# Kernel optimization log

Measured on AMD Instinct MI355X. Metric: run time of the kernel, lower is better.

The kernel has to match this reference:

```python
import jax, jax.numpy as jnp
import numpy as np

# Canonical topology: root object with K arrays, each array has L number leaves.
# Weights are tied across paths (tie_weights_containers=tie_weights_primitives=True),
# NumberEmbedder runs in eval mode with initial buffers mean=0, sqmean=1 -> identity norm.

K, L, D = 8192, 128, 64


def setup_inputs() -> dict:
    key = jax.random.key(0)
    ks = jax.random.split(key, 16)
    s = 1.0 / np.sqrt(D)
    return {
        "x": jax.random.normal(ks[0], (K, L), dtype=jnp.float32),
        "W_num": jax.random.normal(ks[1], (D, 1), dtype=jnp.float32) * s,
        "b_num": jax.random.normal(ks[2], (D,), dtype=jnp.float32) * s,
        "W_ih": jax.random.normal(ks[3], (4 * D, 2 * D), dtype=jnp.float32) * s,
        "W_hh": jax.random.normal(ks[4], (4 * D, D), dtype=jnp.float32) * s,
        "b_ih": jax.random.normal(ks[5], (4 * D,), dtype=jnp.float32) * s,
        "b_hh": jax.random.normal(ks[6], (4 * D,), dtype=jnp.float32) * s,
        "W_aout": jax.random.normal(ks[7], (D, D), dtype=jnp.float32) * s,
        "b_aout": jax.random.normal(ks[8], (D,), dtype=jnp.float32) * s,
        "W_fh": jax.random.normal(ks[9], (D, D), dtype=jnp.float32) * s,
        "b_fh": jax.random.normal(ks[10], (D,), dtype=jnp.float32) * s,
        "W_iouh": jax.random.normal(ks[11], (3 * D, D), dtype=jnp.float32) * s,
        "b_iouh": jax.random.normal(ks[12], (3 * D,), dtype=jnp.float32) * s,
        "W_oout": jax.random.normal(ks[13], (D, D), dtype=jnp.float32) * s,
        "b_oout": jax.random.normal(ks[14], (D,), dtype=jnp.float32) * s,
    }


def _forward(x, W_num, b_num, W_ih, W_hh, b_ih, b_hh, W_aout, b_aout,
             W_fh, b_fh, W_iouh, b_iouh, W_oout, b_oout):
    d = W_hh.shape[1]
    # --- NumberEmbedder: Linear(1, d) on identity-normalized numbers; c = 0 ---
    emb = x[..., None] * W_num[:, 0] + b_num          # [K, L, d]
    xs = jnp.transpose(emb, (1, 0, 2))                # [L, K, d] time-major for scan
    # --- ArrayEmbedder: LSTMCell over children; input = cat(child_h, child_c) ---
    # child_c is identically zero, so only the first half of W_ih contributes.
    W_ih_h = W_ih[:, :d]                              # [4d, d]
    bias = b_ih + b_hh                                # [4d]

    def step(carry, x_t):
        h, c = carry
        gates = x_t @ W_ih_h.T + h @ W_hh.T + bias    # [K, 4d]
        i, f, g, o = jnp.split(gates, 4, axis=1)
        c2 = jax.nn.sigmoid(f) * c + jax.nn.sigmoid(i) * jnp.tanh(g)
        h2 = jax.nn.sigmoid(o) * jnp.tanh(c2)
        return (h2, c2), None

    h0 = jnp.zeros((x.shape[0], d), dtype=x.dtype)
    (h_arr, c_arr), _ = jax.lax.scan(step, (h0, h0), xs)
    h_hat = h_arr @ W_aout.T + b_aout                 # [K, d] array lout
    # --- ObjectEmbedder: child-sum TreeLSTM over the K array states ---
    f = h_hat @ W_fh.T + b_fh                         # [K, d]
    fc_sum = jnp.sum(jax.nn.sigmoid(f) * c_arr, axis=0, keepdims=True)  # [1, d]
    hs_bar = jnp.sum(h_hat, axis=0, keepdims=True)    # [1, d]
    iou = hs_bar @ W_iouh.T + b_iouh                  # [1, 3d]
    i, o, u = jnp.split(iou, 3, axis=1)
    c_obj = jax.nn.sigmoid(i) * jnp.tanh(u) + fc_sum
    h_obj = jax.nn.sigmoid(o) * jnp.tanh(c_obj)
    h_hat_obj = h_obj @ W_oout.T + b_oout             # [1, d] object lout
    # root forward returns cat(h, c)
    return jnp.concatenate([h_hat_obj, c_obj], axis=1)  # [1, 2d]


def reference(x, W_num, b_num, W_ih, W_hh, b_ih, b_hh, W_aout, b_aout,
              W_fh, b_fh, W_iouh, b_iouh, W_oout, b_oout):
    return _forward(x, W_num, b_num, W_ih, W_hh, b_ih, b_hh, W_aout, b_aout,
                    W_fh, b_fh, W_iouh, b_iouh, W_oout, b_oout)
```

## Files before the change

### kernel.cpp

```cpp
#include <hip/hip_runtime.h>
#include <cstddef>

#define D   64
#define L   128
#define NT  256
#define ROWS 16
#define XSS 132
#define HBS 72
#define NBLK 512
#define LOG2E 1.4426950408889634f

typedef __attribute__((ext_vector_type(8))) short short8;
typedef __attribute__((ext_vector_type(4))) float floatx4;

__device__ __forceinline__ float fast_rcp(float x) {
#if defined(__has_builtin)
#if __has_builtin(__builtin_amdgcn_rcpf)
  return __builtin_amdgcn_rcpf(x);
#else
  return 1.0f / x;
#endif
#else
  return 1.0f / x;
#endif
}
__device__ __forceinline__ float ex2(float x) {
#if defined(__has_builtin)
#if __has_builtin(__builtin_amdgcn_exp2f)
  return __builtin_amdgcn_exp2f(x);
#else
  return __builtin_exp2f(x);
#endif
#else
  return __builtin_exp2f(x);
#endif
}
__device__ __forceinline__ float sig_plain(float x) {
  return fast_rcp(1.0f + ex2(-LOG2E * x));
}
__device__ __forceinline__ float tanh2(float G) {
  return fmaf(2.0f, fast_rcp(1.0f + ex2(G)), -1.0f);
}
__device__ __forceinline__ unsigned short f2bf_rtne(float f) {
  unsigned int u = __float_as_uint(f);
  u += 0x7fffu + ((u >> 16) & 1u);
  return (unsigned short)(u >> 16);
}
__device__ __forceinline__ float bf2f(unsigned short s) {
  return __uint_as_float(((unsigned int)s) << 16);
}

__global__ __launch_bounds__(NT, 2)
void lstm_main(const float* __restrict__ x,
               const float* __restrict__ W_num,
               const float* __restrict__ b_num,
               const float* __restrict__ W_ih,
               const float* __restrict__ W_hh,
               const float* __restrict__ b_ih,
               const float* __restrict__ b_hh,
               const float* __restrict__ W_aout,
               const float* __restrict__ b_aout,
               const float* __restrict__ W_fh,
               const float* __restrict__ b_fh,
               const float* __restrict__ W_iouh,
               const float* __restrict__ b_iouh,
               const float* __restrict__ W_oout,
               const float* __restrict__ b_oout,
               float* __restrict__ acc_out,
               float* __restrict__ out)
{
  __shared__ __align__(16) float xs[ROWS * XSS];
  __shared__ __align__(16) short hb[2][ROWS * HBS];
  __shared__ float sacc[2 * D];
  __shared__ float hobj[D];
  __shared__ int   is_last;

  const int tid  = threadIdx.x;
  const int w    = tid >> 6;
  const int lane = tid & 63;
  const int quad = lane >> 4;
  const int c16  = lane & 15;
  const int k0   = blockIdx.x * ROWS;
  const int dcol = w * 16 + c16;

  for (int i = tid; i < ROWS * (L / 4); i += NT) {
    int r = i >> 5, c4 = i & 31;
    float4 v = ((const float4*)(x + (size_t)(k0 + r) * L))[c4];
    float* dst = &xs[r * XSS + c4 * 4];
    dst[0] = v.x; dst[1] = v.y; dst[2] = v.z; dst[3] = v.w;
  }
  for (int i = tid; i < ROWS * HBS; i += NT) hb[0][i] = 0;

  const float gscale[4] = {-LOG2E, -LOG2E, -2.0f * LOG2E, -LOG2E};

  float An[4], Bc[4];
#pragma unroll
  for (int g = 0; g < 4; ++g) {
    int j = g * 64 + dcol;
    const float4* wr = (const float4*)(W_ih + (size_t)j * (2 * D));
    float a = 0.0f, b = b_ih[j] + b_hh[j];
#pragma unroll
    for (int e4 = 0; e4 < 16; ++e4) {
      float4 wv = wr[e4];
      float4 wn = ((const float4*)W_num)[e4];
      float4 bn = ((const float4*)b_num)[e4];
      a = fmaf(wn.x, wv.x, a); a = fmaf(wn.y, wv.y, a);
      a = fmaf(wn.z, wv.z, a); a = fmaf(wn.w, wv.w, a);
      b = fmaf(bn.x, wv.x, b); b = fmaf(bn.y, wv.y, b);
      b = fmaf(bn.z, wv.z, b); b = fmaf(bn.w, wv.w, b);
    }
    An[g] = a * gscale[g]; Bc[g] = b * gscale[g];
  }

  short8 Bhi[4][2], Blo[4][2];
#pragma unroll
  for (int g = 0; g < 4; ++g) {
#pragma unroll
    for (int kk = 0; kk < 2; ++kk) {
      const float4* wp = (const float4*)(W_hh + (size_t)(g * 64 + dcol) * D
                                         + kk * 32 + quad * 8);
      float wv[8];
      float4 w0 = wp[0], w1 = wp[1];
      wv[0]=w0.x; wv[1]=w0.y; wv[2]=w0.z; wv[3]=w0.w;
      wv[4]=w1.x; wv[5]=w1.y; wv[6]=w1.z; wv[7]=w1.w;
      short8 hi8, lo8;
#pragma unroll
      for (int j = 0; j < 8; ++j) {
        float v = wv[j] * gscale[g];
        unsigned short h = f2bf_rtne(v);
        hi8[j] = (short)h;
        lo8[j] = (short)f2bf_rtne(v - bf2f(h));
      }
      Bhi[g][kk] = hi8; Blo[g][kk] = lo8;
    }
  }

  float creg[4] = {0.f, 0.f, 0.f, 0.f};
  float hreg[4] = {0.f, 0.f, 0.f, 0.f};
  __syncthreads();

  int p = 0;
  for (int t4 = 0; t4 < L; t4 += 4) {
    float4 xq[4];
#pragma unroll
    for (int r = 0; r < 4; ++r)
      xq[r] = *(const float4*)&xs[(quad * 4 + r) * XSS + t4];
#pragma unroll
    for (int u = 0; u < 4; ++u) {
      short8 ahi[2];
#pragma unroll
      for (int kk = 0; kk < 2; ++kk)
        ahi[kk] = *(const short8*)&hb[p][c16 * HBS + kk * 32 + quad * 8];
      float xv[4] = {xq[0][u], xq[1][u], xq[2][u], xq[3][u]};
      floatx4 acc[4];
#pragma unroll
      for (int g = 0; g < 4; ++g)
        acc[g] = (floatx4){fmaf(An[g], xv[0], Bc[g]), fmaf(An[g], xv[1], Bc[g]),
                           fmaf(An[g], xv[2], Bc[g]), fmaf(An[g], xv[3], Bc[g])};
#pragma unroll
      for (int kk = 0; kk < 2; ++kk) {
#pragma unroll
        for (int g = 0; g < 4; ++g) {
          acc[g] = __builtin_amdgcn_mfma_f32_16x16x32_bf16(ahi[kk], Bhi[g][kk], acc[g], 0, 0, 0);
          acc[g] = __builtin_amdgcn_mfma_f32_16x16x32_bf16(ahi[kk], Blo[g][kk], acc[g], 0, 0, 0);
        }
      }
#pragma unroll
      for (int r = 0; r < 4; ++r) {
        float Ei = ex2(acc[0][r]);
        float Ef = ex2(acc[1][r]);
        float Eg = ex2(acc[2][r]);
        float Eo = ex2(acc[3][r]);
        float pf = 1.0f + Ef, pi = 1.0f + Ei, pg = 1.0f + Eg;
        float mg = 1.0f - Eg;
        float pig = pi * pg;
        float num = fmaf(creg[r], pig, mg * pf);
        float c2  = num * fast_rcp(pf * pig);
        float Ec  = ex2(-2.0f * LOG2E * c2);
        float po = 1.0f + Eo, pc = 1.0f + Ec, mc = 1.0f - Ec;
        float h2 = mc * fast_rcp(po * pc);
        creg[r] = c2;
        hreg[r] = h2;
        int row = quad * 4 + r;
        hb[p ^ 1][row * HBS + dcol] = (short)f2bf_rtne(h2);
      }
      __syncthreads();
      p ^= 1;
    }
  }

#pragma unroll
  for (int r = 0; r < 4; ++r) xs[(quad * 4 + r) * XSS + dcol] = hreg[r];
  __syncthreads();

  float hhat[4];
#pragma unroll
  for (int r = 0; r < 4; ++r) {
    float a = b_aout[dcol];
    const float4* wa = (const float4*)(W_aout + (size_t)dcol * D);
    const float* hp = &xs[(quad * 4 + r) * XSS];
#pragma unroll
    for (int e4 = 0; e4 < 16; ++e4) {
      float4 wv = wa[e4];
      a = fmaf(wv.x, hp[e4*4+0], a); a = fmaf(wv.y, hp[e4*4+1], a);
      a = fmaf(wv.z, hp[e4*4+2], a); a = fmaf(wv.w, hp[e4*4+3], a);
    }
    hhat[r] = a;
  }
  __syncthreads();
#pragma unroll
  for (int r = 0; r < 4; ++r) xs[(quad * 4 + r) * XSS + 64 + dcol] = hhat[r];
  __syncthreads();

  float pfc = 0.0f, phs = 0.0f;
#pragma unroll
  for (int r = 0; r < 4; ++r) {
    float f = b_fh[dcol];
    const float4* wf = (const float4*)(W_fh + (size_t)dcol * D);
    const float* hp = &xs[(quad * 4 + r) * XSS + 64];
#pragma unroll
    for (int e4 = 0; e4 < 16; ++e4) {
      float4 wv = wf[e4];
      f = fmaf(wv.x, hp[e4*4+0], f); f = fmaf(wv.y, hp[e4*4+1], f);
      f = fmaf(wv.z, hp[e4*4+2], f); f = fmaf(wv.w, hp[e4*4+3], f);
    }
    pfc = fmaf(sig_plain(f), creg[r], pfc);
    phs += hhat[r];
  }
  pfc += __shfl_xor(pfc, 16); pfc += __shfl_xor(pfc, 32);
  phs += __shfl_xor(phs, 16); phs += __shfl_xor(phs, 32);
  if (quad == 0) {
    atomicAdd(acc_out + dcol, pfc);
    atomicAdd(acc_out + D + dcol, phs);
  }

  __threadfence();
  if (tid == 0) {
    unsigned int prev = __hip_atomic_fetch_add((unsigned int*)(acc_out + 2 * D), 1u,
                                               __ATOMIC_ACQ_REL, __HIP_MEMORY_SCOPE_AGENT);
    is_last = (prev == NBLK - 1) ? 1 : 0;
  }
  __syncthreads();
  if (!is_last) return;
  __threadfence();
  if (tid < 2 * D)
    sacc[tid] = __hip_atomic_load(acc_out + tid, __ATOMIC_RELAXED, __HIP_MEMORY_SCOPE_AGENT);
  __syncthreads();
  if (tid < D) {
    const int d = tid;
    float vi = b_iouh[d], vo = b_iouh[D + d], vu = b_iouh[2 * D + d];
    for (int e = 0; e < D; ++e) {
      float hs = sacc[D + e];
      vi = fmaf(W_iouh[(size_t)d * D + e],           hs, vi);
      vo = fmaf(W_iouh[(size_t)(D + d) * D + e],     hs, vo);
      vu = fmaf(W_iouh[(size_t)(2 * D + d) * D + e], hs, vu);
    }
    float c_obj = sig_plain(vi) * tanh2(-2.0f * LOG2E * vu) + sacc[d];
    float h_obj = sig_plain(vo) * tanh2(-2.0f * LOG2E * c_obj);
    hobj[d] = h_obj;
    out[D + d] = c_obj;
  }
  __syncthreads();
  if (tid < D) {
    const int d = tid;
    float hh = b_oout[d];
    for (int e = 0; e < D; ++e) hh = fmaf(W_oout[(size_t)d * D + e], hobj[e], hh);
    out[d] = hh;
  }
}

extern "C" void kernel_launch(void* const* d_in, const int* in_sizes, int n_in,
                              void* d_out, int out_size, void* d_ws, size_t ws_size,
                              hipStream_t stream) {
  const float* x      = (const float*)d_in[0];
  const float* W_num  = (const float*)d_in[1];
  const float* b_num  = (const float*)d_in[2];
  const float* W_ih   = (const float*)d_in[3];
  const float* W_hh   = (const float*)d_in[4];
  const float* b_ih   = (const float*)d_in[5];
  const float* b_hh   = (const float*)d_in[6];
  const float* W_aout = (const float*)d_in[7];
  const float* b_aout = (const float*)d_in[8];
  const float* W_fh   = (const float*)d_in[9];
  const float* b_fh   = (const float*)d_in[10];
  const float* W_iouh = (const float*)d_in[11];
  const float* b_iouh = (const float*)d_in[12];
  const float* W_oout = (const float*)d_in[13];
  const float* b_oout = (const float*)d_in[14];
  float* acc = (float*)d_ws;
  float* out = (float*)d_out;

  hipMemsetAsync(d_ws, 0, (2 * D + 1) * sizeof(float), stream);
  lstm_main<<<NBLK, NT, 0, stream>>>(x, W_num, b_num, W_ih, W_hh, b_ih, b_hh,
                                     W_aout, b_aout, W_fh, b_fh,
                                     W_iouh, b_iouh, W_oout, b_oout, acc, out);
}
```

Before: 218.6 us.

## Split LSTM gates across 8 waves with LDS gate exchange per step

Doubles the block to 512 threads so each wave computes MFMAs for only two of the four gates, halving per-wave MFMA and weight-register load. Gate pre-activations are written to a padded LDS buffer and redistributed so each thread handles the elementwise cell update for two (row, column) pairs. The epilogue reductions now go through shared-memory atomics before the global ones. The cost is an extra __syncthreads and an LDS round-trip on every timestep of the serial recurrence.

```diff
diff --git a/kernel.cpp b/kernel.cpp
--- a/kernel.cpp
+++ b/kernel.cpp
@@ -3,10 +3,11 @@
 
 #define D   64
 #define L   128
-#define NT  256
+#define NT  512
 #define ROWS 16
 #define XSS 132
 #define HBS 72
+#define GS  17
 #define NBLK 512
 #define LOG2E 1.4426950408889634f
 
@@ -50,7 +51,7 @@
   return __uint_as_float(((unsigned int)s) << 16);
 }
 
-__global__ __launch_bounds__(NT, 2)
+__global__ __launch_bounds__(NT, 4)
 void lstm_main(const float* __restrict__ x,
                const float* __restrict__ W_num,
                const float* __restrict__ b_num,
@@ -70,6 +71,7 @@
                float* __restrict__ out)
 {
   __shared__ __align__(16) float xs[ROWS * XSS];
+  __shared__ __align__(16) float gbuf[4 * 64 * GS];
   __shared__ __align__(16) short hb[2][ROWS * HBS];
   __shared__ float sacc[2 * D];
   __shared__ float hobj[D];
@@ -77,11 +79,16 @@
 
   const int tid  = threadIdx.x;
   const int w    = tid >> 6;
+  const int wq   = w & 3;
+  const int wg   = w >> 2;
   const int lane = tid & 63;
   const int quad = lane >> 4;
   const int c16  = lane & 15;
   const int k0   = blockIdx.x * ROWS;
-  const int dcol = w * 16 + c16;
+  const int dcol = wq * 16 + c16;
+  const int erow = 2 * w + (lane >> 5);
+  const int dd0  = lane & 31;
+  const int dd1  = dd0 + 32;
 
   for (int i = tid; i < ROWS * (L / 4); i += NT) {
     int r = i >> 5, c4 = i & 31;
@@ -90,12 +97,14 @@
     dst[0] = v.x; dst[1] = v.y; dst[2] = v.z; dst[3] = v.w;
   }
   for (int i = tid; i < ROWS * HBS; i += NT) hb[0][i] = 0;
+  if (tid < 2 * D) sacc[tid] = 0.0f;
 
   const float gscale[4] = {-LOG2E, -LOG2E, -2.0f * LOG2E, -LOG2E};
 
-  float An[4], Bc[4];
-#pragma unroll
-  for (int g = 0; g < 4; ++g) {
+  float An[2], Bc[2];
+#pragma unroll
+  for (int gl = 0; gl < 2; ++gl) {
+    int g = 2 * wg + gl;
     int j = g * 64 + dcol;
     const float4* wr = (const float4*)(W_ih + (size_t)j * (2 * D));
     float a = 0.0f, b = b_ih[j] + b_hh[j];
@@ -109,12 +118,13 @@
       b = fmaf(bn.x, wv.x, b); b = fmaf(bn.y, wv.y, b);
       b = fmaf(bn.z, wv.z, b); b = fmaf(bn.w, wv.w, b);
     }
-    An[g] = a * gscale[g]; Bc[g] = b * gscale[g];
-  }
-
-  short8 Bhi[4][2], Blo[4][2];
-#pragma unroll
-  for (int g = 0; g < 4; ++g) {
+    An[gl] = a * gscale[g]; Bc[gl] = b * gscale[g];
+  }
+
+  short8 Bhi[2][2], Blo[2][2];
+#pragma unroll
+  for (int gl = 0; gl < 2; ++gl) {
+    int g = 2 * wg + gl;
 #pragma unroll
     for (int kk = 0; kk < 2; ++kk) {
       const float4* wp = (const float4*)(W_hh + (size_t)(g * 64 + dcol) * D
@@ -131,12 +141,12 @@
         hi8[j] = (short)h;
         lo8[j] = (short)f2bf_rtne(v - bf2f(h));
       }
-      Bhi[g][kk] = hi8; Blo[g][kk] = lo8;
-    }
-  }
-
-  float creg[4] = {0.f, 0.f, 0.f, 0.f};
-  float hreg[4] = {0.f, 0.f, 0.f, 0.f};
+      Bhi[gl][kk] = hi8; Blo[gl][kk] = lo8;
+    }
+  }
+
+  float c0 = 0.0f, c1 = 0.0f;
+  float h0 = 0.0f, h1 = 0.0f;
   __syncthreads();
 
   int p = 0;
@@ -152,87 +162,108 @@
       for (int kk = 0; kk < 2; ++kk)
         ahi[kk] = *(const short8*)&hb[p][c16 * HBS + kk * 32 + quad * 8];
       float xv[4] = {xq[0][u], xq[1][u], xq[2][u], xq[3][u]};
-      floatx4 acc[4];
-#pragma unroll
-      for (int g = 0; g < 4; ++g)
-        acc[g] = (floatx4){fmaf(An[g], xv[0], Bc[g]), fmaf(An[g], xv[1], Bc[g]),
-                           fmaf(An[g], xv[2], Bc[g]), fmaf(An[g], xv[3], Bc[g])};
+      floatx4 acc[2];
+#pragma unroll
+      for (int gl = 0; gl < 2; ++gl)
+        acc[gl] = (floatx4){fmaf(An[gl], xv[0], Bc[gl]), fmaf(An[gl], xv[1], Bc[gl]),
+                            fmaf(An[gl], xv[2], Bc[gl]), fmaf(An[gl], xv[3], Bc[gl])};
 #pragma unroll
       for (int kk = 0; kk < 2; ++kk) {
 #pragma unroll
-        for (int g = 0; g < 4; ++g) {
-          acc[g] = __builtin_amdgcn_mfma_f32_16x16x32_bf16(ahi[kk], Bhi[g][kk], acc[g], 0, 0, 0);
-          acc[g] = __builtin_amdgcn_mfma_f32_16x16x32_bf16(ahi[kk], Blo[g][kk], acc[g], 0, 0, 0);
+        for (int gl = 0; gl < 2; ++gl) {
+          acc[gl] = __builtin_amdgcn_mfma_f32_16x16x32_bf16(ahi[kk], Bhi[gl][kk], acc[gl], 0, 0, 0);
+          acc[gl] = __builtin_amdgcn_mfma_f32_16x16x32_bf16(ahi[kk], Blo[gl][kk], acc[gl], 0, 0, 0);
         }
       }
 #pragma unroll
-      for (int r = 0; r < 4; ++r) {
-        float Ei = ex2(acc[0][r]);
-        float Ef = ex2(acc[1][r]);
-        float Eg = ex2(acc[2][r]);
-        float Eo = ex2(acc[3][r]);
-        float pf = 1.0f + Ef, pi = 1.0f + Ei, pg = 1.0f + Eg;
-        float mg = 1.0f - Eg;
-        float pig = pi * pg;
-        float num = fmaf(creg[r], pig, mg * pf);
-        float c2  = num * fast_rcp(pf * pig);
-        float Ec  = ex2(-2.0f * LOG2E * c2);
-        float po = 1.0f + Eo, pc = 1.0f + Ec, mc = 1.0f - Ec;
-        float h2 = mc * fast_rcp(po * pc);
-        creg[r] = c2;
-        hreg[r] = h2;
-        int row = quad * 4 + r;
-        hb[p ^ 1][row * HBS + dcol] = (short)f2bf_rtne(h2);
+      for (int gl = 0; gl < 2; ++gl) {
+        int gbase = ((2 * wg + gl) * 64 + dcol) * GS + quad * 4;
+#pragma unroll
+        for (int r = 0; r < 4; ++r) gbuf[gbase + r] = acc[gl][r];
+      }
+      __syncthreads();
+      {
+        float Gi0 = gbuf[(0 * 64 + dd0) * GS + erow];
+        float Gf0 = gbuf[(1 * 64 + dd0) * GS + erow];
+        float Gg0 = gbuf[(2 * 64 + dd0) * GS + erow];
+        float Go0 = gbuf[(3 * 64 + dd0) * GS + erow];
+        float Gi1 = gbuf[(0 * 64 + dd1) * GS + erow];
+        float Gf1 = gbuf[(1 * 64 + dd1) * GS + erow];
+        float Gg1 = gbuf[(2 * 64 + dd1) * GS + erow];
+        float Go1 = gbuf[(3 * 64 + dd1) * GS + erow];
+        float Ei0 = ex2(Gi0), Ef0 = ex2(Gf0), Eg0 = ex2(Gg0), Eo0 = ex2(Go0);
+        float Ei1 = ex2(Gi1), Ef1 = ex2(Gf1), Eg1 = ex2(Gg1), Eo1 = ex2(Go1);
+        float pf0 = 1.0f + Ef0, pi0 = 1.0f + Ei0, pg0 = 1.0f + Eg0, mg0 = 1.0f - Eg0;
+        float pf1 = 1.0f + Ef1, pi1 = 1.0f + Ei1, pg1 = 1.0f + Eg1, mg1 = 1.0f - Eg1;
+        float pig0 = pi0 * pg0, pig1 = pi1 * pg1;
+        float nc0 = fmaf(c0, pig0, mg0 * pf0);
+        float nc1 = fmaf(c1, pig1, mg1 * pf1);
+        c0 = nc0 * fast_rcp(pf0 * pig0);
+        c1 = nc1 * fast_rcp(pf1 * pig1);
+        float Ec0 = ex2(-2.0f * LOG2E * c0);
+        float Ec1 = ex2(-2.0f * LOG2E * c1);
+        h0 = (1.0f - Ec0) * fast_rcp((1.0f + Eo0) * (1.0f + Ec0));
+        h1 = (1.0f - Ec1) * fast_rcp((1.0f + Eo1) * (1.0f + Ec1));
+        short* hw = &hb[p ^ 1][erow * HBS];
+        hw[dd0] = (short)f2bf_rtne(h0);
+        hw[dd1] = (short)f2bf_rtne(h1);
       }
       __syncthreads();
       p ^= 1;
     }
   }
 
-#pragma unroll
-  for (int r = 0; r < 4; ++r) xs[(quad * 4 + r) * XSS + dcol] = hreg[r];
-  __syncthreads();
-
-  float hhat[4];
-#pragma unroll
-  for (int r = 0; r < 4; ++r) {
-    float a = b_aout[dcol];
-    const float4* wa = (const float4*)(W_aout + (size_t)dcol * D);
-    const float* hp = &xs[(quad * 4 + r) * XSS];
+  xs[erow * XSS + dd0] = h0;
+  xs[erow * XSS + dd1] = h1;
+  __syncthreads();
+
+  float hh0 = b_aout[dd0], hh1 = b_aout[dd1];
+  {
+    const float4* wa0 = (const float4*)(W_aout + (size_t)dd0 * D);
+    const float4* wa1 = (const float4*)(W_aout + (size_t)dd1 * D);
+    const float* hp = &xs[erow * XSS];
 #pragma unroll
     for (int e4 = 0; e4 < 16; ++e4) {
-      float4 wv = wa[e4];
-      a = fmaf(wv.x, hp[e4*4+0], a); a = fmaf(wv.y, hp[e4*4+1], a);
-      a = fmaf(wv.z, hp[e4*4+2], a); a = fmaf(wv.w, hp[e4*4+3], a);
-    }
-    hhat[r] = a;
-  }
-  __syncthreads();
-#pragma unroll
-  for (int r = 0; r < 4; ++r) xs[(quad * 4 + r) * XSS + 64 + dcol] = hhat[r];
-  __syncthreads();
-
-  float pfc = 0.0f, phs = 0.0f;
-#pragma unroll
-  for (int r = 0; r < 4; ++r) {
-    float f = b_fh[dcol];
-    const float4* wf = (const float4*)(W_fh + (size_t)dcol * D);
-    const float* hp = &xs[(quad * 4 + r) * XSS + 64];
+      float4 v0 = wa0[e4], v1 = wa1[e4];
+      float p0 = hp[e4*4+0], p1 = hp[e4*4+1], p2 = hp[e4*4+2], p3 = hp[e4*4+3];
+      hh0 = fmaf(v0.x, p0, hh0); hh0 = fmaf(v0.y, p1, hh0);
+      hh0 = fmaf(v0.z, p2, hh0); hh0 = fmaf(v0.w, p3, hh0);
+      hh1 = fmaf(v1.x, p0, hh1); hh1 = fmaf(v1.y, p1, hh1);
+      hh1 = fmaf(v1.z, p2, hh1); hh1 = fmaf(v1.w, p3, hh1);
+    }
+  }
+  xs[erow * XSS + 64 + dd0] = hh0;
+  xs[erow * XSS + 64 + dd1] = hh1;
+  __syncthreads();
+
+  float f0 = b_fh[dd0], f1 = b_fh[dd1];
+  {
+    const float4* wf0 = (const float4*)(W_fh + (size_t)dd0 * D);
+    const float4* wf1 = (const float4*)(W_fh + (size_t)dd1 * D);
+    const float* hp = &xs[erow * XSS + 64];
 #pragma unroll
     for (int e4 = 0; e4 < 16; ++e4) {
-      float4 wv = wf[e4];
-      f = fmaf(wv.x, hp[e4*4+0], f); f = fmaf(wv.y, hp[e4*4+1], f);
-      f = fmaf(wv.z, hp[e4*4+2], f); f = fmaf(wv.w, hp[e4*4+3], f);
-    }
-    pfc = fmaf(sig_plain(f), creg[r], pfc);
-    phs += hhat[r];
-  }
-  pfc += __shfl_xor(pfc, 16); pfc += __shfl_xor(pfc, 32);
-  phs += __shfl_xor(phs, 16); phs += __shfl_xor(phs, 32);
-  if (quad == 0) {
-    atomicAdd(acc_out + dcol, pfc);
-    atomicAdd(acc_out + D + dcol, phs);
-  }
+      float4 v0 = wf0[e4], v1 = wf1[e4];
+      float p0 = hp[e4*4+0], p1 = hp[e4*4+1], p2 = hp[e4*4+2], p3 = hp[e4*4+3];
+      f0 = fmaf(v0.x, p0, f0); f0 = fmaf(v0.y, p1, f0);
+      f0 = fmaf(v0.z, p2, f0); f0 = fmaf(v0.w, p3, f0);
+      f1 = fmaf(v1.x, p0, f1); f1 = fmaf(v1.y, p1, f1);
+      f1 = fmaf(v1.z, p2, f1); f1 = fmaf(v1.w, p3, f1);
+    }
+  }
+  float pfc0 = sig_plain(f0) * c0, pfc1 = sig_plain(f1) * c1;
+  float phs0 = hh0, phs1 = hh1;
+  pfc0 += __shfl_xor(pfc0, 32); pfc1 += __shfl_xor(pfc1, 32);
+  phs0 += __shfl_xor(phs0, 32); phs1 += __shfl_xor(phs1, 32);
+  if (lane < 32) {
+    atomicAdd(&sacc[dd0], pfc0);
+    atomicAdd(&sacc[dd1], pfc1);
+    atomicAdd(&sacc[D + dd0], phs0);
+    atomicAdd(&sacc[D + dd1], phs1);
+  }
+  __syncthreads();
+  if (tid < 2 * D) atomicAdd(acc_out + tid, sacc[tid]);
+  __syncthreads();
 
   __threadfence();
   if (tid == 0) {
```

Measured after the change: 272.6 us. 24.7% more time.
